# Kernel tuning notes

Hardware: AMD Instinct MI355X
Metric: run time of the kernel (lower is better)

Reference implementation:

```python
import jax, jax.numpy as jnp
import numpy as np

N_TIMESTEPS = 50
IN_DIM = 4 * 64 * 64  # in_channels * image_size^2
OUT_CH = 2
BATCH = 4096


def setup_inputs() -> dict:
    key = jax.random.key(0)
    k_x, k_t, k_w, k_b = jax.random.split(key, 4)
    x = jax.random.normal(k_x, (BATCH, 4, 64, 64), dtype=jnp.float32)
    # t holds actual diffusion timesteps drawn from TIMESTEPS = [980, 960, ..., 0]
    t_idx = jax.random.randint(k_t, (BATCH,), 0, N_TIMESTEPS)
    t = (980 - 20 * t_idx).astype(jnp.int64)
    # stacked per-timestep Linear params (nn.Linear default init ~ U(-1/sqrt(in), 1/sqrt(in)))
    bound = 1.0 / np.sqrt(IN_DIM)
    W = jax.random.uniform(k_w, (N_TIMESTEPS, OUT_CH, IN_DIM), dtype=jnp.float32, minval=-bound, maxval=bound)
    b = jax.random.uniform(k_b, (N_TIMESTEPS, OUT_CH), dtype=jnp.float32, minval=-bound, maxval=bound)
    return {"x": x, "t": t, "W": W, "b": b}


def reference(x, t, W, b):
    B = x.shape[0]
    xf = x.reshape(B, -1)  # [B, IN_DIM]
    # TIMESTEPS.index(ti): TIMESTEPS[i] = 980 - 20*i  ->  i = (980 - ti) // 20
    idx = (980 - t) // 20  # [B]
    Wg = W[idx]  # [B, OUT_CH, IN_DIM] (per-sample gathered weights, as in torch.stack)
    bg = b[idx]  # [B, OUT_CH]
    # bmm(x[:,None,:], Wg^T).squeeze(1) + bias
    out = jnp.einsum('bi,boi->bo', xf, Wg) + bg
    return out
```

## Files before the change

kernel.cpp:

```cpp
#include <hip/hip_runtime.h>

constexpr int IN_DIM  = 4 * 64 * 64;
constexpr int OUT_CH  = 2;
constexpr int NT      = 50;
constexpr int BLOCK   = 256;
constexpr int NGROUPS = IN_DIM / 4;
constexpr int ITERS   = NGROUPS / BLOCK;
constexpr size_t WB_BYTES = (size_t)NT * OUT_CH * IN_DIM * 2;

typedef float fx4 __attribute__((ext_vector_type(4)));

__device__ __forceinline__ unsigned short f2bf_rn(float f) {
    unsigned int u = __float_as_uint(f);
    u += 0x7FFFu + ((u >> 16) & 1u);
    return (unsigned short)(u >> 16);
}

__global__ __launch_bounds__(BLOCK) void convert_w_kernel(
    const float* __restrict__ W, unsigned short* __restrict__ Wb)
{
    const int g = blockIdx.x * BLOCK + threadIdx.x;
    if (g >= NT * NGROUPS) return;
    const int ts = g / NGROUPS;
    const int j  = g - ts * NGROUPS;
    const float* base = W + (size_t)ts * OUT_CH * IN_DIM;
    const float4 a = *reinterpret_cast<const float4*>(base + j * 4);
    const float4 c = *reinterpret_cast<const float4*>(base + IN_DIM + j * 4);
    ushort4 lo, hi;
    lo.x = f2bf_rn(a.x); lo.y = f2bf_rn(a.y); lo.z = f2bf_rn(a.z); lo.w = f2bf_rn(a.w);
    hi.x = f2bf_rn(c.x); hi.y = f2bf_rn(c.y); hi.z = f2bf_rn(c.z); hi.w = f2bf_rn(c.w);
    ushort4* dst = reinterpret_cast<ushort4*>(Wb + (size_t)ts * OUT_CH * IN_DIM) + (size_t)j * 2;
    dst[0] = lo;
    dst[1] = hi;
}

__global__ __launch_bounds__(BLOCK) void dot_bf16w_kernel(
    const float* __restrict__ x,
    const int*   __restrict__ t,
    const unsigned short* __restrict__ Wb,
    const float* __restrict__ bias,
    float*       __restrict__ out)
{
    const int b   = blockIdx.x;
    const int tid = threadIdx.x;
    const int idx = (980 - t[b]) / 20;

    const fx4*   xv = reinterpret_cast<const fx4*>(x + (size_t)b * IN_DIM);
    const uint4* wv = reinterpret_cast<const uint4*>(Wb + (size_t)idx * OUT_CH * IN_DIM);

    float e0 = 0.0f, e1 = 0.0f, o0 = 0.0f, o1 = 0.0f;
#pragma unroll
    for (int i = 0; i < ITERS; i += 2) {
        const int j0 = tid + i * BLOCK;
        const int j1 = tid + (i + 1) * BLOCK;
        const fx4 xa = __builtin_nontemporal_load(&xv[j0]);
        const fx4 xb = __builtin_nontemporal_load(&xv[j1]);
        const uint4 wa = wv[j0];
        const uint4 wb = wv[j1];

        e0 += xa.x * __uint_as_float(wa.x << 16)
            + xa.y * __uint_as_float(wa.x & 0xFFFF0000u)
            + xa.z * __uint_as_float(wa.y << 16)
            + xa.w * __uint_as_float(wa.y & 0xFFFF0000u);
        e1 += xa.x * __uint_as_float(wa.z << 16)
            + xa.y * __uint_as_float(wa.z & 0xFFFF0000u)
            + xa.z * __uint_as_float(wa.w << 16)
            + xa.w * __uint_as_float(wa.w & 0xFFFF0000u);

        o0 += xb.x * __uint_as_float(wb.x << 16)
            + xb.y * __uint_as_float(wb.x & 0xFFFF0000u)
            + xb.z * __uint_as_float(wb.y << 16)
            + xb.w * __uint_as_float(wb.y & 0xFFFF0000u);
        o1 += xb.x * __uint_as_float(wb.z << 16)
            + xb.y * __uint_as_float(wb.z & 0xFFFF0000u)
            + xb.z * __uint_as_float(wb.w << 16)
            + xb.w * __uint_as_float(wb.w & 0xFFFF0000u);
    }
    float acc0 = e0 + o0;
    float acc1 = e1 + o1;

    for (int off = 32; off > 0; off >>= 1) {
        acc0 += __shfl_down(acc0, off, 64);
        acc1 += __shfl_down(acc1, off, 64);
    }

    __shared__ float red[BLOCK / 64][2];
    const int wave = tid >> 6;
    if ((tid & 63) == 0) {
        red[wave][0] = acc0;
        red[wave][1] = acc1;
    }
    __syncthreads();

    if (tid == 0) {
        float s0 = red[0][0] + red[1][0] + red[2][0] + red[3][0];
        float s1 = red[0][1] + red[1][1] + red[2][1] + red[3][1];
        out[(size_t)b * OUT_CH + 0] = s0 + bias[idx * OUT_CH + 0];
        out[(size_t)b * OUT_CH + 1] = s1 + bias[idx * OUT_CH + 1];
    }
}

__global__ __launch_bounds__(BLOCK) void dot_f32_kernel(
    const float* __restrict__ x, const int* __restrict__ t,
    const float* __restrict__ W, const float* __restrict__ bias,
    float* __restrict__ out)
{
    const int b   = blockIdx.x;
    const int tid = threadIdx.x;
    const int idx = (980 - t[b]) / 20;

    const float4* xv = reinterpret_cast<const float4*>(x + (size_t)b * IN_DIM);
    const float4* w0 = reinterpret_cast<const float4*>(W + (size_t)idx * OUT_CH * IN_DIM);
    const float4* w1 = w0 + IN_DIM / 4;

    float acc0 = 0.0f, acc1 = 0.0f;
#pragma unroll
    for (int i = 0; i < ITERS; ++i) {
        const int j = tid + i * BLOCK;
        const float4 xv4 = xv[j];
        const float4 a   = w0[j];
        const float4 c   = w1[j];
        acc0 += xv4.x * a.x + xv4.y * a.y + xv4.z * a.z + xv4.w * a.w;
        acc1 += xv4.x * c.x + xv4.y * c.y + xv4.z * c.z + xv4.w * c.w;
    }
    for (int off = 32; off > 0; off >>= 1) {
        acc0 += __shfl_down(acc0, off, 64);
        acc1 += __shfl_down(acc1, off, 64);
    }
    __shared__ float red[BLOCK / 64][2];
    const int wave = tid >> 6;
    if ((tid & 63) == 0) { red[wave][0] = acc0; red[wave][1] = acc1; }
    __syncthreads();
    if (tid == 0) {
        float s0 = red[0][0] + red[1][0] + red[2][0] + red[3][0];
        float s1 = red[0][1] + red[1][1] + red[2][1] + red[3][1];
        out[(size_t)b * OUT_CH + 0] = s0 + bias[idx * OUT_CH + 0];
        out[(size_t)b * OUT_CH + 1] = s1 + bias[idx * OUT_CH + 1];
    }
}

extern "C" void kernel_launch(void* const* d_in, const int* in_sizes, int n_in,
                              void* d_out, int out_size, void* d_ws, size_t ws_size,
                              hipStream_t stream) {
    const float* x    = (const float*)d_in[0];
    const int*   t    = (const int*)d_in[1];
    const float* W    = (const float*)d_in[2];
    const float* bias = (const float*)d_in[3];
    float*       out  = (float*)d_out;
    const int B = in_sizes[1];

    if (ws_size >= WB_BYTES) {
        unsigned short* Wb = (unsigned short*)d_ws;
        const int ngrp = NT * NGROUPS;
        convert_w_kernel<<<(ngrp + BLOCK - 1) / BLOCK, BLOCK, 0, stream>>>(W, Wb);
        dot_bf16w_kernel<<<B, BLOCK, 0, stream>>>(x, t, Wb, bias, out);
    } else {
        dot_f32_kernel<<<B, BLOCK, 0, stream>>>(x, t, W, bias, out);
    }
}
```

Baseline: 58.24 us.

## Stage gathered bf16 weights in shared memory and double block size

The dot kernel first copies the selected timestep's bf16 weight row into 64KB of LDS, syncs, then streams x against the LDS copy. The block size doubles to 512. The convert kernel now handles two groups per thread with nontemporal loads. Each weight element is still read only once per block, so the staging brings no reuse. It adds a barrier and heavy LDS use, which limits blocks per CU.

```diff
diff --git a/kernel.cpp b/kernel.cpp
--- a/kernel.cpp
+++ b/kernel.cpp
@@ -3,7 +3,7 @@
 constexpr int IN_DIM  = 4 * 64 * 64;
 constexpr int OUT_CH  = 2;
 constexpr int NT      = 50;
-constexpr int BLOCK   = 256;
+constexpr int BLOCK   = 512;
 constexpr int NGROUPS = IN_DIM / 4;
 constexpr int ITERS   = NGROUPS / BLOCK;
 constexpr size_t WB_BYTES = (size_t)NT * OUT_CH * IN_DIM * 2;
@@ -16,22 +16,26 @@
     return (unsigned short)(u >> 16);
 }
 
-__global__ __launch_bounds__(BLOCK) void convert_w_kernel(
+__global__ __launch_bounds__(256) void convert_w_kernel(
     const float* __restrict__ W, unsigned short* __restrict__ Wb)
 {
-    const int g = blockIdx.x * BLOCK + threadIdx.x;
-    if (g >= NT * NGROUPS) return;
-    const int ts = g / NGROUPS;
-    const int j  = g - ts * NGROUPS;
-    const float* base = W + (size_t)ts * OUT_CH * IN_DIM;
-    const float4 a = *reinterpret_cast<const float4*>(base + j * 4);
-    const float4 c = *reinterpret_cast<const float4*>(base + IN_DIM + j * 4);
-    ushort4 lo, hi;
-    lo.x = f2bf_rn(a.x); lo.y = f2bf_rn(a.y); lo.z = f2bf_rn(a.z); lo.w = f2bf_rn(a.w);
-    hi.x = f2bf_rn(c.x); hi.y = f2bf_rn(c.y); hi.z = f2bf_rn(c.z); hi.w = f2bf_rn(c.w);
-    ushort4* dst = reinterpret_cast<ushort4*>(Wb + (size_t)ts * OUT_CH * IN_DIM) + (size_t)j * 2;
-    dst[0] = lo;
-    dst[1] = hi;
+    const int g0 = (blockIdx.x * 256 + threadIdx.x) * 2;
+    if (g0 >= NT * NGROUPS) return;
+#pragma unroll
+    for (int k = 0; k < 2; ++k) {
+        const int g  = g0 + k;
+        const int ts = g / NGROUPS;
+        const int j  = g - ts * NGROUPS;
+        const float* base = W + (size_t)ts * OUT_CH * IN_DIM;
+        const fx4 a = __builtin_nontemporal_load(reinterpret_cast<const fx4*>(base + j * 4));
+        const fx4 c = __builtin_nontemporal_load(reinterpret_cast<const fx4*>(base + IN_DIM + j * 4));
+        ushort4 lo, hi;
+        lo.x = f2bf_rn(a.x); lo.y = f2bf_rn(a.y); lo.z = f2bf_rn(a.z); lo.w = f2bf_rn(a.w);
+        hi.x = f2bf_rn(c.x); hi.y = f2bf_rn(c.y); hi.z = f2bf_rn(c.z); hi.w = f2bf_rn(c.w);
+        ushort4* dst = reinterpret_cast<ushort4*>(Wb + (size_t)ts * OUT_CH * IN_DIM) + (size_t)j * 2;
+        dst[0] = lo;
+        dst[1] = hi;
+    }
 }
 
 __global__ __launch_bounds__(BLOCK) void dot_bf16w_kernel(
@@ -41,6 +45,8 @@
     const float* __restrict__ bias,
     float*       __restrict__ out)
 {
+    __shared__ uint4 wsm[NGROUPS];
+
     const int b   = blockIdx.x;
     const int tid = threadIdx.x;
     const int idx = (980 - t[b]) / 20;
@@ -48,15 +54,22 @@
     const fx4*   xv = reinterpret_cast<const fx4*>(x + (size_t)b * IN_DIM);
     const uint4* wv = reinterpret_cast<const uint4*>(Wb + (size_t)idx * OUT_CH * IN_DIM);
 
+#pragma unroll
+    for (int k = 0; k < ITERS; ++k) {
+        const int j = tid + k * BLOCK;
+        wsm[j] = wv[j];
+    }
+    __syncthreads();
+
     float e0 = 0.0f, e1 = 0.0f, o0 = 0.0f, o1 = 0.0f;
 #pragma unroll
     for (int i = 0; i < ITERS; i += 2) {
         const int j0 = tid + i * BLOCK;
         const int j1 = tid + (i + 1) * BLOCK;
-        const fx4 xa = __builtin_nontemporal_load(&xv[j0]);
-        const fx4 xb = __builtin_nontemporal_load(&xv[j1]);
-        const uint4 wa = wv[j0];
-        const uint4 wb = wv[j1];
+        const fx4  xa = __builtin_nontemporal_load(&xv[j0]);
+        const fx4  xb = __builtin_nontemporal_load(&xv[j1]);
+        const uint4 wa = wsm[j0];
+        const uint4 wb = wsm[j1];
 
         e0 += xa.x * __uint_as_float(wa.x << 16)
             + xa.y * __uint_as_float(wa.x & 0xFFFF0000u)
@@ -93,14 +106,15 @@
     __syncthreads();
 
     if (tid == 0) {
-        float s0 = red[0][0] + red[1][0] + red[2][0] + red[3][0];
-        float s1 = red[0][1] + red[1][1] + red[2][1] + red[3][1];
+        float s0 = 0.0f, s1 = 0.0f;
+#pragma unroll
+        for (int w = 0; w < BLOCK / 64; ++w) { s0 += red[w][0]; s1 += red[w][1]; }
         out[(size_t)b * OUT_CH + 0] = s0 + bias[idx * OUT_CH + 0];
         out[(size_t)b * OUT_CH + 1] = s1 + bias[idx * OUT_CH + 1];
     }
 }
 
-__global__ __launch_bounds__(BLOCK) void dot_f32_kernel(
+__global__ __launch_bounds__(256) void dot_f32_kernel(
     const float* __restrict__ x, const int* __restrict__ t,
     const float* __restrict__ W, const float* __restrict__ bias,
     float* __restrict__ out)
@@ -115,8 +129,8 @@
 
     float acc0 = 0.0f, acc1 = 0.0f;
 #pragma unroll
-    for (int i = 0; i < ITERS; ++i) {
-        const int j = tid + i * BLOCK;
+    for (int i = 0; i < 16; ++i) {
+        const int j = tid + i * 256;
         const float4 xv4 = xv[j];
         const float4 a   = w0[j];
         const float4 c   = w1[j];
@@ -127,7 +141,7 @@
         acc0 += __shfl_down(acc0, off, 64);
         acc1 += __shfl_down(acc1, off, 64);
     }
-    __shared__ float red[BLOCK / 64][2];
+    __shared__ float red[4][2];
     const int wave = tid >> 6;
     if ((tid & 63) == 0) { red[wave][0] = acc0; red[wave][1] = acc1; }
     __syncthreads();
@@ -151,10 +165,10 @@
 
     if (ws_size >= WB_BYTES) {
         unsigned short* Wb = (unsigned short*)d_ws;
-        const int ngrp = NT * NGROUPS;
-        convert_w_kernel<<<(ngrp + BLOCK - 1) / BLOCK, BLOCK, 0, stream>>>(W, Wb);
+        const int nthreads = NT * NGROUPS / 2;
+        convert_w_kernel<<<(nthreads + 255) / 256, 256, 0, stream>>>(W, Wb);
         dot_bf16w_kernel<<<B, BLOCK, 0, stream>>>(x, t, Wb, bias, out);
     } else {
-        dot_f32_kernel<<<B, BLOCK, 0, stream>>>(x, t, W, bias, out);
+        dot_f32_kernel<<<B, 256, 0, stream>>>(x, t, W, bias, out);
     }
 }
```

Result: slower. 60.01 us (+3.0%).
